# Kernel optimization log

Hardware: AMD Instinct MI355X
Metric: run time of the kernel (lower is better)

Reference implementation:

```python
import jax, jax.numpy as jnp
import numpy as np

K, N, M = 65536, 4096, 64  # observations, basis centers, features


def setup_inputs() -> dict:
    key = jax.random.key(0)
    k1, k2, k3, k4 = jax.random.split(key, 4)
    x = jax.random.normal(k1, (K, M), dtype=jnp.float32)
    x_basis = jax.random.normal(k2, (N, M), dtype=jnp.float32)
    w = jax.random.normal(k3, (1, N), dtype=jnp.float32) / np.sqrt(N)
    b = jax.random.normal(k4, (1,), dtype=jnp.float32)
    return {"x": x, "x_basis": x_basis, "w": w, "b": b}


def reference(x, x_basis, w, b):
    # pairwise squared distances ||x_i - c_j||^2, [K, N]
    x2 = jnp.sum(x * x, axis=1, keepdims=True)          # [K, 1]
    c2 = jnp.sum(x_basis * x_basis, axis=1)             # [N]
    sq = x2 + c2[None, :] - 2.0 * (x @ x_basis.T)       # [K, N]
    phi = jnp.exp(-sq)                                  # gaussian RBF
    return jax.nn.sigmoid(phi @ w.T + b)                # [K, 1]
```

## Files before the change

### kernel.cpp

```cpp
#include <hip/hip_runtime.h>


#define KOBS 65536
#define NCENT 4096
#define MFEAT 64
#define NCHUNK 32

#define SCALE_A 2.8853900817779268f
#define QS      1.4426950408889634f
#define TSKIP   -60.0f

typedef __attribute__((ext_vector_type(4)))  float float4v;
typedef __attribute__((ext_vector_type(16))) float float16v;
typedef __attribute__((ext_vector_type(8)))  int   int8v;

#if __has_builtin(__builtin_amdgcn_exp2f)
#define EXP2F(x) __builtin_amdgcn_exp2f(x)
#else
#define EXP2F(x) exp2f(x)
#endif

static __device__ inline unsigned f2bfu(float f) {
    unsigned u = __float_as_uint(f);
    return (u + 0x7fffu + ((u >> 16) & 1u)) >> 16;
}

#define MFMA(A, B, C) __builtin_amdgcn_mfma_scale_f32_32x32x64_f8f6f4( \
    (A), (B), (C), 0, 0, 0, 0x7f7f7f7f, 0, 0x7f7f7f7f)

__global__ __launch_bounds__(256) void rbf_prep(
    const float* __restrict__ xb, const float* __restrict__ w,
    char* __restrict__ cb, unsigned* __restrict__ hcw) {
    const int bid = blockIdx.x;
    const int tid = threadIdx.x;
    if (bid < 128) {
        const int o      = bid * 256 + tid;
        const int col    = o >> 3;
        const int joct   = o & 7;
        const int c      = col >> 7;
        const int w4     = (col >> 5) & 3;
        const int lanelo = col & 31;
        const int l      = lanelo + (joct >> 2) * 32;
        const int j0     = (joct & 3) * 8;
        const float* src = xb + col * MFEAT + joct * 8;
        float4v v0 = *(const float4v*)(src);
        float4v v1 = *(const float4v*)(src + 4);
        int lo = __builtin_amdgcn_cvt_pk_fp8_f32(v0[0], v0[1], 0, false);
        lo     = __builtin_amdgcn_cvt_pk_fp8_f32(v0[2], v0[3], lo, true);
        int hi = __builtin_amdgcn_cvt_pk_fp8_f32(v1[0], v1[1], 0, false);
        hi     = __builtin_amdgcn_cvt_pk_fp8_f32(v1[2], v1[3], hi, true);
        unsigned long long pk = (unsigned long long)(unsigned)lo |
                                ((unsigned long long)(unsigned)hi << 32);
        *(unsigned long long*)(cb + (size_t)((c * 4 + w4) * 64 + l) * 32 + j0) = pk;
    } else {
        const int row  = (bid - 128) * 4 + (tid >> 6);
        const int lane = tid & 63;
        float v = xb[row * MFEAT + lane];
        float s = v * v;
        #pragma unroll
        for (int off = 32; off > 0; off >>= 1) s += __shfl_xor(s, off, 64);
        if (lane == 0)
            hcw[row] = (f2bfu(TSKIP + QS * s) << 16) | f2bfu(w[row]);
    }
}

__global__ __launch_bounds__(512, 4) void rbf_main(
    const float* __restrict__ x, const char* __restrict__ cb,
    const unsigned* __restrict__ hcw, const float* __restrict__ bptr,
    float* __restrict__ out) {
    __shared__ float x2s[128];
    __shared__ float zl[128];

    const int tid  = threadIdx.x;
    const int wv   = tid >> 6;
    const int lane = tid & 63;
    const int ll   = lane & 31;
    const int lh   = lane >> 5;
    const int rt   = wv >> 2;
    const int wq   = wv & 3;
    const int bid  = (int)blockIdx.x;

    if (tid < 128) zl[tid] = 0.0f;

    const int r0e = bid * 128 + rt * 64;
    int8v af0, af1;
    #pragma unroll
    for (int t = 0; t < 2; ++t) {
        const float* xr = x + (size_t)(r0e + t * 32 + ll) * MFEAT + lh * 32;
        int8v a;
        float ss = 0.0f;
        #pragma unroll
        for (int rg = 0; rg < 8; ++rg) {
            float4v v = *(const float4v*)(xr + rg * 4);
            ss = fmaf(v[0], v[0], ss); ss = fmaf(v[1], v[1], ss);
            ss = fmaf(v[2], v[2], ss); ss = fmaf(v[3], v[3], ss);
            int pk = __builtin_amdgcn_cvt_pk_fp8_f32(
                SCALE_A * v[0], SCALE_A * v[1], 0, false);
            pk = __builtin_amdgcn_cvt_pk_fp8_f32(
                SCALE_A * v[2], SCALE_A * v[3], pk, true);
            a[rg] = pk;
        }
        ss += __shfl_xor(ss, 32, 64);
        if (t == 0) af0 = a; else af1 = a;
        if (wq == 0 && lh == 0) x2s[rt * 64 + t * 32 + ll] = ss;
    }
    __syncthreads();

    const int rb = 4 * lh;
    float16v p0, p1;
    #pragma unroll
    for (int i = 0; i < 16; ++i) {
        const int ri = rb + (i & 3) + 8 * (i >> 2);
        p0[i] = -QS * x2s[rt * 64 + ri];
        p1[i] = -QS * x2s[rt * 64 + 32 + ri];
    }

    const int zbase = rt * 64 + rb;
    const unsigned cboff = (unsigned)(wq * 64 + lane) * 32u;
    const unsigned moff  = (unsigned)(wq * 32 + ll);

    int8v    pb[3];
    unsigned mw[3];

    #define LOADB(C, S) do {                                               \
        pb[S] = *(const int8v*)(cb + cboff + (unsigned)(C) * 8192u);       \
        mw[S] = hcw[moff + (unsigned)(C) * 128u];                          \
    } while (0)

    #define STEP(C, SCUR, SPRE, DOLOAD) do {                               \
        if (DOLOAD) LOADB((C) + 2, SPRE);                                  \
        float16v a0 = MFMA(af0, pb[SCUR], p0);                             \
        float16v a1 = MFMA(af1, pb[SCUR], p1);                             \
        const unsigned mu = mw[SCUR];                                      \
        const float tq  = __uint_as_float(mu & 0xffff0000u);               \
        const float wv_ = __uint_as_float(mu << 16);                       \
        float uA0 = fmaxf(fmaxf(a0[0],  a0[1]),  a0[2]);                   \
        float uA1 = fmaxf(fmaxf(a0[3],  a0[4]),  a0[5]);                   \
        float uA2 = fmaxf(fmaxf(a0[6],  a0[7]),  a0[8]);                   \
        float uA3 = fmaxf(fmaxf(a0[9],  a0[10]), a0[11]);                  \
        float uA4 = fmaxf(fmaxf(a0[12], a0[13]), a0[14]);                  \
        float mA  = fmaxf(fmaxf(fmaxf(uA0, uA1), uA2),                     \
                          fmaxf(fmaxf(uA3, uA4), a0[15]));                 \
        float uB0 = fmaxf(fmaxf(a1[0],  a1[1]),  a1[2]);                   \
        float uB1 = fmaxf(fmaxf(a1[3],  a1[4]),  a1[5]);                   \
        float uB2 = fmaxf(fmaxf(a1[6],  a1[7]),  a1[8]);                   \
        float uB3 = fmaxf(fmaxf(a1[9],  a1[10]), a1[11]);                  \
        float uB4 = fmaxf(fmaxf(a1[12], a1[13]), a1[14]);                  \
        float mB  = fmaxf(fmaxf(fmaxf(uB0, uB1), uB2),                     \
                          fmaxf(fmaxf(uB3, uB4), a1[15]));                 \
        if (__any(fmaxf(mA, mB) > tq)) {         \
            const float q = TSKIP - tq;              \
            if (mA > tq) {                                                 \
                _Pragma("unroll")                                          \
                for (int i_ = 0; i_ < 16; ++i_)                            \
                    atomicAdd(&zl[zbase + (i_ & 3) + 8 * (i_ >> 2)],       \
                              wv_ * EXP2F(a0[i_] + q));                    \
            }                                                              \
            if (mB > tq) {                                                 \
                _Pragma("unroll")                                          \
                for (int i_ = 0; i_ < 16; ++i_)                            \
                    atomicAdd(&zl[zbase + 32 + (i_ & 3) + 8 * (i_ >> 2)],  \
                              wv_ * EXP2F(a1[i_] + q));                    \
            }                                                              \
        }                                                                  \
    } while (0)

    LOADB(0, 0);
    LOADB(1, 1);

    #pragma unroll 1
    for (int c = 0; c < 30; c += 3) {
        STEP(c,     0, 2, 1);
        STEP(c + 1, 1, 0, 1);
        STEP(c + 2, 2, 1, 1);
    }
    STEP(30, 0, 2, 0);
    STEP(31, 1, 0, 0);

    #undef STEP
    #undef LOADB

    __syncthreads();
    if (tid < 128) {
        const float z = zl[tid] + bptr[0];
        out[bid * 128 + tid] = 1.0f / (1.0f + EXP2F(-QS * z));
    }
}

extern "C" void kernel_launch(void* const* d_in, const int* in_sizes, int n_in,
                              void* d_out, int out_size, void* d_ws, size_t ws_size,
                              hipStream_t stream) {
    const float* x  = (const float*)d_in[0];
    const float* xb = (const float*)d_in[1];
    const float* w  = (const float*)d_in[2];
    const float* b  = (const float*)d_in[3];
    float* out = (float*)d_out;

    char*     cb  = (char*)d_ws;
    unsigned* hcw = (unsigned*)((char*)d_ws + NCENT * MFEAT);

    rbf_prep<<<128 + NCENT / 4, 256, 0, stream>>>(xb, w, cb, hcw);
    rbf_main<<<KOBS / 128, 512, 0, stream>>>(x, cb, hcw, b, out);
}
```

Measured before the change: 88.23 us.

## Halve rows per block and drop accumulator bias to raise occupancy

Each block now handles 64 observations with one fp8 MFMA per center chunk instead of two. The -x² bias is no longer preloaded into the MFMA accumulator. The skip test uses a conservative per-wave minimum of x², and the exact per-row bias is applied only inside the exp path. Prefetching drops from three buffers to two and launch bounds request 8 waves, all to cut VGPR use and raise occupancy. In exchange the grid doubles, so every center tile is read twice as often from cache, and the looser skip threshold may run the exp/atomic path more often.

```diff
diff --git a/kernel.cpp b/kernel.cpp
--- a/kernel.cpp
+++ b/kernel.cpp
@@ -4,7 +4,6 @@
 #define KOBS 65536
 #define NCENT 4096
 #define MFEAT 64
-#define NCHUNK 32
 
 #define SCALE_A 2.8853900817779268f
 #define QS      1.4426950408889634f
@@ -64,12 +63,12 @@
     }
 }
 
-__global__ __launch_bounds__(512, 4) void rbf_main(
+__global__ __launch_bounds__(512, 8) void rbf_main(
     const float* __restrict__ x, const char* __restrict__ cb,
     const unsigned* __restrict__ hcw, const float* __restrict__ bptr,
     float* __restrict__ out) {
-    __shared__ float x2s[128];
-    __shared__ float zl[128];
+    __shared__ float x2s[64];
+    __shared__ float zl[64];
 
     const int tid  = threadIdx.x;
     const int wv   = tid >> 6;
@@ -79,15 +78,14 @@
     const int rt   = wv >> 2;
     const int wq   = wv & 3;
     const int bid  = (int)blockIdx.x;
+    const int rt32 = rt * 32;
+    const int rb   = 4 * lh;
 
-    if (tid < 128) zl[tid] = 0.0f;
+    if (tid < 64) zl[tid] = 0.0f;
 
-    const int r0e = bid * 128 + rt * 64;
-    int8v af0, af1;
-    #pragma unroll
-    for (int t = 0; t < 2; ++t) {
-        const float* xr = x + (size_t)(r0e + t * 32 + ll) * MFEAT + lh * 32;
-        int8v a;
+    int8v af;
+    {
+        const float* xr = x + (size_t)(bid * 64 + rt32 + ll) * MFEAT + lh * 32;
         float ss = 0.0f;
         #pragma unroll
         for (int rg = 0; rg < 8; ++rg) {
@@ -98,92 +96,84 @@
                 SCALE_A * v[0], SCALE_A * v[1], 0, false);
             pk = __builtin_amdgcn_cvt_pk_fp8_f32(
                 SCALE_A * v[2], SCALE_A * v[3], pk, true);
-            a[rg] = pk;
+            af[rg] = pk;
         }
         ss += __shfl_xor(ss, 32, 64);
-        if (t == 0) af0 = a; else af1 = a;
-        if (wq == 0 && lh == 0) x2s[rt * 64 + t * 32 + ll] = ss;
+        if (wq == 0 && lh == 0) x2s[rt32 + ll] = ss;
     }
     __syncthreads();
 
-    const int rb = 4 * lh;
-    float16v p0, p1;
-    #pragma unroll
-    for (int i = 0; i < 16; ++i) {
-        const int ri = rb + (i & 3) + 8 * (i >> 2);
-        p0[i] = -QS * x2s[rt * 64 + ri];
-        p1[i] = -QS * x2s[rt * 64 + 32 + ri];
+    float pmx;
+    {
+        float pv = x2s[rt32 + ll];
+        pv = fminf(pv, __shfl_xor(pv, 1,  64));
+        pv = fminf(pv, __shfl_xor(pv, 2,  64));
+        pv = fminf(pv, __shfl_xor(pv, 4,  64));
+        pv = fminf(pv, __shfl_xor(pv, 8,  64));
+        pv = fminf(pv, __shfl_xor(pv, 16, 64));
+        pmx = -QS * pv;
     }
 
-    const int zbase = rt * 64 + rb;
     const unsigned cboff = (unsigned)(wq * 64 + lane) * 32u;
     const unsigned moff  = (unsigned)(wq * 32 + ll);
 
-    int8v    pb[3];
-    unsigned mw[3];
+    int8v    pb[2];
+    unsigned mw[2];
 
     #define LOADB(C, S) do {                                               \
         pb[S] = *(const int8v*)(cb + cboff + (unsigned)(C) * 8192u);       \
         mw[S] = hcw[moff + (unsigned)(C) * 128u];                          \
     } while (0)
 
-    #define STEP(C, SCUR, SPRE, DOLOAD) do {                               \
-        if (DOLOAD) LOADB((C) + 2, SPRE);                                  \
-        float16v a0 = MFMA(af0, pb[SCUR], p0);                             \
-        float16v a1 = MFMA(af1, pb[SCUR], p1);                             \
-        const unsigned mu = mw[SCUR];                                      \
-        const float tq  = __uint_as_float(mu & 0xffff0000u);               \
-        const float wv_ = __uint_as_float(mu << 16);                       \
-        float uA0 = fmaxf(fmaxf(a0[0],  a0[1]),  a0[2]);                   \
-        float uA1 = fmaxf(fmaxf(a0[3],  a0[4]),  a0[5]);                   \
-        float uA2 = fmaxf(fmaxf(a0[6],  a0[7]),  a0[8]);                   \
-        float uA3 = fmaxf(fmaxf(a0[9],  a0[10]), a0[11]);                  \
-        float uA4 = fmaxf(fmaxf(a0[12], a0[13]), a0[14]);                  \
-        float mA  = fmaxf(fmaxf(fmaxf(uA0, uA1), uA2),                     \
-                          fmaxf(fmaxf(uA3, uA4), a0[15]));                 \
-        float uB0 = fmaxf(fmaxf(a1[0],  a1[1]),  a1[2]);                   \
-        float uB1 = fmaxf(fmaxf(a1[3],  a1[4]),  a1[5]);                   \
-        float uB2 = fmaxf(fmaxf(a1[6],  a1[7]),  a1[8]);                   \
-        float uB3 = fmaxf(fmaxf(a1[9],  a1[10]), a1[11]);                  \
-        float uB4 = fmaxf(fmaxf(a1[12], a1[13]), a1[14]);                  \
-        float mB  = fmaxf(fmaxf(fmaxf(uB0, uB1), uB2),                     \
-                          fmaxf(fmaxf(uB3, uB4), a1[15]));                 \
-        if (__any(fmaxf(mA, mB) > tq)) {         \
-            const float q = TSKIP - tq;              \
-            if (mA > tq) {                                                 \
-                _Pragma("unroll")                                          \
-                for (int i_ = 0; i_ < 16; ++i_)                            \
-                    atomicAdd(&zl[zbase + (i_ & 3) + 8 * (i_ >> 2)],       \
-                              wv_ * EXP2F(a0[i_] + q));                    \
-            }                                                              \
-            if (mB > tq) {                                                 \
-                _Pragma("unroll")                                          \
-                for (int i_ = 0; i_ < 16; ++i_)                            \
-                    atomicAdd(&zl[zbase + 32 + (i_ & 3) + 8 * (i_ >> 2)],  \
-                              wv_ * EXP2F(a1[i_] + q));                    \
-            }                                                              \
-        }                                                                  \
+    #define STEP(C, S, DOLOAD) do {                                       \
+        const unsigned mu = mw[S];                                        \
+        const float tq  = __uint_as_float(mu & 0xffff0000u);              \
+        const float wv_ = __uint_as_float(mu << 16);                      \
+        float16v d;                                                       \
+        _Pragma("unroll")                                                 \
+        for (int z_ = 0; z_ < 16; ++z_) d[z_] = 0.0f;                     \
+        d = MFMA(af, pb[S], d);                                           \
+        if (DOLOAD) LOADB((C) + 2, S);                                    \
+        float u0 = fmaxf(fmaxf(d[0],  d[1]),  d[2]);                      \
+        float u1 = fmaxf(fmaxf(d[3],  d[4]),  d[5]);                      \
+        float u2 = fmaxf(fmaxf(d[6],  d[7]),  d[8]);                      \
+        float u3 = fmaxf(fmaxf(d[9],  d[10]), d[11]);                     \
+        float u4 = fmaxf(fmaxf(d[12], d[13]), d[14]);                     \
+        float mxd = fmaxf(fmaxf(fmaxf(u0, u1), u2),                       \
+                          fmaxf(fmaxf(u3, u4), d[15]));                   \
+        const float thr = tq - pmx;              \
+        if (__any(mxd > thr)) {                       \
+            const float q = TSKIP - tq;             \
+            if (mxd > thr) {                                              \
+                _Pragma("unroll")                                         \
+                for (int i_ = 0; i_ < 16; ++i_) {                         \
+                    const int row_ = rb + (i_ & 3) + 8 * (i_ >> 2);       \
+                    const float pi_ = -QS * x2s[rt32 + row_];             \
+                    atomicAdd(&zl[rt32 + row_],                           \
+                              wv_ * EXP2F(d[i_] + pi_ + q));              \
+                }                                                         \
+            }                                                             \
+        }                                                                 \
     } while (0)
 
     LOADB(0, 0);
     LOADB(1, 1);
 
     #pragma unroll 1
-    for (int c = 0; c < 30; c += 3) {
-        STEP(c,     0, 2, 1);
-        STEP(c + 1, 1, 0, 1);
-        STEP(c + 2, 2, 1, 1);
+    for (int c = 0; c < 30; c += 2) {
+        STEP(c,     0, 1);
+        STEP(c + 1, 1, 1);
     }
-    STEP(30, 0, 2, 0);
-    STEP(31, 1, 0, 0);
+    STEP(30, 0, 0);
+    STEP(31, 1, 0);
 
     #undef STEP
     #undef LOADB
 
     __syncthreads();
-    if (tid < 128) {
+    if (tid < 64) {
         const float z = zl[tid] + bptr[0];
-        out[bid * 128 + tid] = 1.0f / (1.0f + EXP2F(-QS * z));
+        out[bid * 64 + tid] = 1.0f / (1.0f + EXP2F(-QS * z));
     }
 }
 
@@ -200,5 +190,5 @@
     unsigned* hcw = (unsigned*)((char*)d_ws + NCENT * MFEAT);
 
     rbf_prep<<<128 + NCENT / 4, 256, 0, stream>>>(xb, w, cb, hcw);
-    rbf_main<<<KOBS / 128, 512, 0, stream>>>(x, cb, hcw, b, out);
+    rbf_main<<<KOBS / 64, 512, 0, stream>>>(x, cb, hcw, b, out);
 }
```

After: 104.8 us. 18.8% more time.
